# Performance work log

Measured on AMD Instinct MI355X. Metric: run time of the kernel, lower is better.

The kernel has to match this reference:

```python
import jax, jax.numpy as jnp
import numpy as np
from jax import lax

B, C, HW = 256, 3, 64
D, K, LAT = 256, 8192, 128  # embedding_dim, num_embeddings, latent per head
EPS = 1e-5
SLOPE = 0.01  # LeakyReLU default
DN = ('NCHW', 'OIHW', 'NCHW')

def _conv(x, w, b, s, p):
    y = lax.conv_general_dilated(x, w, (s, s), ((p, p), (p, p)), dimension_numbers=DN)
    return y + b[None, :, None, None]

def _convT(x, w, b, s, p, op):
    # PyTorch ConvTranspose2d weight is (Cin, Cout, kh, kw): flip spatial, swap io.
    wt = jnp.flip(w, (2, 3)).transpose(1, 0, 2, 3)
    lo = w.shape[2] - 1 - p
    y = lax.conv_general_dilated(x, wt, (1, 1), ((lo, lo + op), (lo, lo + op)),
                                 lhs_dilation=(s, s), dimension_numbers=DN)
    return y + b[None, :, None, None]

def _bn(x):
    # training-mode BatchNorm2d with default affine init (gamma=1, beta=0)
    mu = jnp.mean(x, (0, 2, 3), keepdims=True)
    var = jnp.var(x, (0, 2, 3), keepdims=True)
    return (x - mu) * lax.rsqrt(var + EPS)

def _lrelu(x):
    return jnp.where(x >= 0, x, SLOPE * x)

def _forward(x, enc_w1, enc_b1, enc_w2, enc_b2, enc_w3, enc_b3, enc_w4, enc_b4,
             enc_wmu, enc_bmu, enc_wcov, enc_bcov, codebook,
             dec_wfc, dec_bfc, dec_wt1, dec_bt1, dec_wt2, dec_bt2,
             dec_wt3, dec_bt3, dec_wt31, dec_bt31, dec_wt4, dec_bt4):
    # ---- Encoder ----
    h = _bn(_lrelu(_conv(x, enc_w1, enc_b1, 2, 1)))   # [B,32,32,32]
    h = _bn(_lrelu(_conv(h, enc_w2, enc_b2, 2, 1)))   # [B,64,16,16]
    h = _bn(_lrelu(_conv(h, enc_w3, enc_b3, 2, 1)))   # [B,128,8,8]
    h = _bn(_lrelu(_conv(h, enc_w4, enc_b4, 2, 1)))   # [B,256,4,4]
    h = h.reshape(h.shape[0], -1)                     # [B,4096]
    mu = h @ enc_wmu.T + enc_bmu                      # [B,LAT]
    cov = jax.nn.relu(h @ enc_wcov.T + enc_bcov)      # [B,LAT]
    z_e = jnp.concatenate([mu, cov], axis=1)          # [B,D]
    # ---- VQ: pairwise L2 -> argmin -> gather ----
    d2 = (jnp.sum(z_e * z_e, 1, keepdims=True)
          + jnp.sum(codebook * codebook, 1)[None, :]
          - 2.0 * (z_e @ codebook.T))                 # [B,K]
    idx = jnp.argmin(d2, axis=1)                      # [B]
    z_q = codebook[idx]                               # [B,D]
    sg = lax.stop_gradient
    emb_loss = jnp.sum((sg(z_e) - z_q) ** 2)
    com_loss = jnp.sum((z_e - sg(z_q)) ** 2)
    vq_loss = emb_loss + com_loss
    z_q_st = z_e + sg(z_q - z_e)                      # straight-through
    # ---- Decoder ----
    g = (z_q_st @ dec_wfc.T + dec_bfc).reshape(-1, 256, 4, 4)
    g = _bn(_lrelu(_convT(g, dec_wt1, dec_bt1, 2, 1, 1)))    # [B,128,8,8]
    g = _bn(_lrelu(_convT(g, dec_wt2, dec_bt2, 2, 1, 1)))    # [B,64,16,16]
    g = _bn(_lrelu(_convT(g, dec_wt3, dec_bt3, 2, 1, 1)))    # [B,32,32,32]
    g = _bn(_lrelu(_convT(g, dec_wt31, dec_bt31, 2, 1, 1)))  # [B,32,64,64]
    out = jnp.tanh(_convT(g, dec_wt4, dec_bt4, 1, 1, 0))     # [B,3,64,64]
    x_hat = 0.5 + 0.5 * out
    return x_hat, vq_loss

def setup_inputs() -> dict:
    key = jax.random.key(0)
    ks = iter(jax.random.split(key, 40))
    def n(shape, s=0.05):
        return (jax.random.normal(next(ks), shape) * s).astype(jnp.float32)
    FC_IN = 256 * 4 * 4
    inp = {
        'x': jax.random.normal(next(ks), (B, C, HW, HW), dtype=jnp.float32),
        'enc_w1': n((32, C, 3, 3)), 'enc_b1': n((32,)),
        'enc_w2': n((64, 32, 3, 3)), 'enc_b2': n((64,)),
        'enc_w3': n((128, 64, 3, 3)), 'enc_b3': n((128,)),
        'enc_w4': n((256, 128, 3, 3)), 'enc_b4': n((256,)),
        'enc_wmu': n((LAT, FC_IN), 0.02), 'enc_bmu': n((LAT,)),
        'enc_wcov': n((LAT, FC_IN), 0.02), 'enc_bcov': n((LAT,)),
        'codebook': jax.random.uniform(next(ks), (K, D), jnp.float32, -1.0 / K, 1.0 / K),
        'dec_wfc': n((FC_IN, D), 0.02), 'dec_bfc': n((FC_IN,)),
        'dec_wt1': n((256, 128, 3, 3)), 'dec_bt1': n((128,)),
        'dec_wt2': n((128, 64, 3, 3)), 'dec_bt2': n((64,)),
        'dec_wt3': n((64, 32, 3, 3)), 'dec_bt3': n((32,)),
        'dec_wt31': n((32, 32, 3, 3)), 'dec_bt31': n((32,)),
        'dec_wt4': n((32, C, 3, 3)), 'dec_bt4': n((C,)),
    }
    return inp

def reference(x, enc_w1, enc_b1, enc_w2, enc_b2, enc_w3, enc_b3, enc_w4, enc_b4,
              enc_wmu, enc_bmu, enc_wcov, enc_bcov, codebook,
              dec_wfc, dec_bfc, dec_wt1, dec_bt1, dec_wt2, dec_bt2,
              dec_wt3, dec_bt3, dec_wt31, dec_bt31, dec_wt4, dec_bt4):
    return _forward(x, enc_w1, enc_b1, enc_w2, enc_b2, enc_w3, enc_b3, enc_w4, enc_b4,
                    enc_wmu, enc_bmu, enc_wcov, enc_bcov, codebook,
                    dec_wfc, dec_bfc, dec_wt1, dec_bt1, dec_wt2, dec_bt2,
                    dec_wt3, dec_bt3, dec_wt31, dec_bt31, dec_wt4, dec_bt4)
```

## Files before the change

kernel.cpp:

```cpp
#include <hip/hip_runtime.h>
#include <cmath>


#define EPS_BN 1e-5f
typedef unsigned short ushort;
typedef short short8 __attribute__((ext_vector_type(8)));
typedef ushort us4 __attribute__((ext_vector_type(4)));
typedef float f32x4 __attribute__((ext_vector_type(4)));

__device__ __forceinline__ float lrelu(float v) { return v >= 0.f ? v : 0.01f * v; }
__device__ __forceinline__ ushort f2bf(float f) {
  unsigned u = __float_as_uint(f);
  return (ushort)((u + 0x7FFF + ((u >> 16) & 1)) >> 16);
}
__device__ __forceinline__ float bf2f(ushort u) {
  return __uint_as_float(((unsigned)u) << 16);
}

__global__ __launch_bounds__(256) void tr_convw_bf(const float* __restrict__ w,
                                                   ushort* __restrict__ wT,
                                                   int CIN, int COUT, int total) {
  int i = blockIdx.x * 256 + threadIdx.x;
  if (i >= total) return;
  int co = i / (9 * CIN);
  int r = i - co * 9 * CIN;
  int t = r / CIN, ci = r - t * CIN;
  wT[i] = f2bf(w[((size_t)co * CIN + ci) * 9 + t]);
}

__global__ __launch_bounds__(256) void tr_convtw_bf(const float* __restrict__ w,
                                                    ushort* __restrict__ wT,
                                                    int CIN, int COUT, int total) {
  int i = blockIdx.x * 256 + threadIdx.x;
  if (i >= total) return;
  const int cc = CIN * COUT;
  int p, base, Kp;
  if (i < cc) { p = 0; base = 0; Kp = CIN; }
  else if (i < 3 * cc) { p = 1; base = cc; Kp = 2 * CIN; }
  else if (i < 5 * cc) { p = 2; base = 3 * cc; Kp = 2 * CIN; }
  else { p = 3; base = 5 * cc; Kp = 4 * CIN; }
  const int r = i - base;
  const int co = r / Kp;
  const int q = r - co * Kp;
  const int tix = q / CIN, ci = q - (q / CIN) * CIN;
  const int py = p >> 1, px = p & 1;
  const int nx = px ? 2 : 1;
  const int kyi = tix / nx, kxi = tix - kyi * nx;
  const int ky = py ? (kyi == 0 ? 0 : 2) : 1;
  const int kx = px ? (kxi == 0 ? 0 : 2) : 1;
  wT[i] = f2bf(w[((size_t)ci * COUT + co) * 9 + ky * 3 + kx]);
}

__global__ __launch_bounds__(256) void tr_convtw_tc(const float* __restrict__ w,
                                                    ushort* __restrict__ wT,
                                                    int CIN, int COUT, int total) {
  int i = blockIdx.x * 256 + threadIdx.x;
  if (i >= total) return;
  int ci = i % CIN;
  int tmp = i / CIN;
  int co = tmp % COUT;
  int t = tmp / COUT;
  const int co_slot = ((co & 1) << 4) | (co >> 1);
  wT[((size_t)t * COUT + co_slot) * CIN + ci] =
      f2bf(w[((size_t)ci * COUT + co) * 9 + t]);
}

__global__ __launch_bounds__(256) void tr_w4(const float* __restrict__ w,
                                             ushort* __restrict__ wT) {
  int i = blockIdx.x * 256 + threadIdx.x;
  if (i >= 4608) return;
  const int s = i >> 9;
  const int l = (i >> 3) & 63;
  const int j = i & 7;
  const int nn = l & 15;
  const int ci = ((l >> 4) << 3) + j;
  const int ty = s / 3, tx = s - ty * 3;
  ushort v = 0;
  if (nn < 3)
    v = f2bf(w[((size_t)ci * 3 + nn) * 9 + (2 - ty) * 3 + (2 - tx)]);
  wT[i] = v;
}

__global__ __launch_bounds__(256) void tr_w1b(const float* __restrict__ w,
                                              ushort* __restrict__ wT) {
  int i = blockIdx.x * 256 + threadIdx.x;
  if (i >= 1024) return;
  const int j = i & 7, l = (i >> 3) & 63, f = i >> 9;
  const int c = 2 * (l & 15) + f;
  const int k = ((l >> 4) << 3) + j;
  ushort v = 0;
  if (k < 27) {
    const int ci = k / 9, r = k - ci * 9;
    v = f2bf(w[((size_t)c * 3 + ci) * 9 + r]);
  }
  wT[i] = v;
}

__global__ __launch_bounds__(256) void tr_a4(const float* __restrict__ in,
                                             float* __restrict__ out) {
  int i = blockIdx.x * 256 + threadIdx.x;
  int n = i >> 12, k = i & 4095;
  out[i] = in[(size_t)(n << 12) + ((k & 15) << 8) + (k >> 4)];
}

__global__ __launch_bounds__(256) void tr_fcdec(const float* __restrict__ in,
                                                const float* __restrict__ bin,
                                                float* __restrict__ out,
                                                float* __restrict__ bout) {
  int i = blockIdx.x * 256 + threadIdx.x;
  int k = i >> 8, d = i & 255;
  int kp = (k & 15) * 256 + (k >> 4);
  out[(size_t)kp * 256 + d] = in[i];
  if (d == 0) bout[kp] = bin[k];
}

template <int TN, int MODE, int IH, int CIN, int COUT, bool HASN, bool INBF>
__global__ __launch_bounds__(256) void mfmaconv(
    const float* __restrict__ X, const ushort* __restrict__ WT,
    const float* __restrict__ bias, const float* __restrict__ st, float invN,
    float* __restrict__ Y, float* __restrict__ stOut) {
  constexpr int OH = (MODE == 0) ? IH / 2 : 2 * IH;
  constexpr int NF = TN / 16;
  __shared__ short As[2][64][40];
  __shared__ short Bs[2][TN][40];
  __shared__ float nrm0[HASN ? CIN : 4], nrm1[HASN ? CIN : 4];
  __shared__ float redS[4][TN], redQ[4][TN];
  const int tid = threadIdx.x;
  const int wv = tid >> 6, lane = tid & 63;
  const int quad = lane >> 4, ln15 = tid & 15;
  if (HASN) {
    for (int c = tid; c < CIN; c += 256) {
      float m = st[c] * invN;
      float var = st[256 + c] * invN - m * m;
      float s = rsqrtf(var + EPS_BN);
      nrm0[c] = s;
      nrm1[c] = m * s;
    }
    __syncthreads();
  }
  int py = 0, px = 0, nx = 1, K = 9 * CIN;
  const ushort* W = WT;
  if (MODE == 1) {
    const int pz = blockIdx.z;
    py = pz >> 1;
    px = pz & 1;
    nx = px ? 2 : 1;
    const int ny = py ? 2 : 1;
    K = ny * nx * CIN;
    const int pre[4] = {0, 1, 3, 5};
    W = WT + (size_t)pre[pz] * CIN * COUT;
  }
  const int gyTM = blockIdx.y * 64;
  const int gxTN = blockIdx.x * TN;

  const int sm = tid & 63, skg = (tid >> 6) * 8;
  const int bn = tid >> 2, bkg = (tid & 3) * 8;
  int baseNB, baseIY, baseIX;
  {
    const int gm = gyTM + sm;
    if (MODE == 0) {
      const int ni = gm / (OH * OH), r = gm % (OH * OH);
      baseNB = ni * IH * IH;
      baseIY = 2 * (r / OH) - 1;
      baseIX = 2 * (r % OH) - 1;
    } else {
      const int ni = gm / (IH * IH), r = gm % (IH * IH);
      baseNB = ni * IH * IH;
      baseIY = r / IH;
      baseIX = r % IH;
    }
  }
  f32x4 acc[NF];
#pragma unroll
  for (int f = 0; f < NF; ++f) acc[f] = (f32x4){0.f, 0.f, 0.f, 0.f};

  const int nsteps = K / 32;

  {
    int iy, ix;
    if (MODE == 0) {
      iy = baseIY;
      ix = baseIX;
    } else {
      iy = baseIY + (py ? 1 : 0);
      ix = baseIX + (px ? 1 : 0);
    }
    const bool ok =
        ((unsigned)iy < (unsigned)IH) && ((unsigned)ix < (unsigned)IH);
    float v[8] = {0.f, 0.f, 0.f, 0.f, 0.f, 0.f, 0.f, 0.f};
    if (ok) {
      if constexpr (INBF) {
        const ushort* xp =
            (const ushort*)X + ((size_t)baseNB + iy * IH + ix) * CIN + skg;
        const short8 raw = *(const short8*)xp;
#pragma unroll
        for (int u = 0; u < 8; ++u) v[u] = bf2f((ushort)raw[u]);
      } else {
        const float* xp = &X[((size_t)baseNB + iy * IH + ix) * CIN + skg];
        const float4 va = *(const float4*)xp, vb = *(const float4*)(xp + 4);
        v[0] = va.x; v[1] = va.y; v[2] = va.z; v[3] = va.w;
        v[4] = vb.x; v[5] = vb.y; v[6] = vb.z; v[7] = vb.w;
      }
      if (HASN) {
#pragma unroll
        for (int u = 0; u < 8; ++u)
          v[u] = fmaf(v[u], nrm0[skg + u], -nrm1[skg + u]);
      }
    }
    short8 o;
#pragma unroll
    for (int u = 0; u < 8; ++u) o[u] = (short)f2bf(v[u]);
    *(short8*)&As[0][sm][skg] = o;
    if (tid < TN * 4)
      *(short8*)&Bs[0][bn][bkg] =
          *(const short8*)&W[(size_t)(gxTN + bn) * K + bkg];
  }
  __syncthreads();

  for (int kk = 0; kk < nsteps; ++kk) {
    const int cur = kk & 1, nxt = cur ^ 1;

    bool okN = false;
    int ci0N = 0;
    short8 rawN;
    float4 vaN, vbN;
    short8 rawBN;
    const bool hasNext = (kk + 1 < nsteps);
    if (hasNext) {
      const int k0n = (kk + 1) * 32;
      const int t = k0n / CIN;
      ci0N = k0n - t * CIN;
      int iy, ix;
      if (MODE == 0) {
        iy = baseIY + t / 3;
        ix = baseIX + (t - (t / 3) * 3);
      } else {
        const int kyi = t / nx, kxi = t - (t / nx) * nx;
        iy = baseIY + ((py && kyi == 0) ? 1 : 0);
        ix = baseIX + ((px && kxi == 0) ? 1 : 0);
      }
      okN = ((unsigned)iy < (unsigned)IH) && ((unsigned)ix < (unsigned)IH);
      if (okN) {
        if constexpr (INBF) {
          const ushort* xp = (const ushort*)X +
                             ((size_t)baseNB + iy * IH + ix) * CIN + ci0N + skg;
          rawN = *(const short8*)xp;
        } else {
          const float* xp =
              &X[((size_t)baseNB + iy * IH + ix) * CIN + ci0N + skg];
          vaN = *(const float4*)xp;
          vbN = *(const float4*)(xp + 4);
        }
      }
      if (tid < TN * 4)
        rawBN = *(const short8*)&W[(size_t)(gxTN + bn) * K + k0n + bkg];
    }

    const short8 a = *(const short8*)&As[cur][wv * 16 + ln15][quad * 8];
#pragma unroll
    for (int f = 0; f < NF; ++f) {
      const short8 b = *(const short8*)&Bs[cur][f * 16 + ln15][quad * 8];
      acc[f] = __builtin_amdgcn_mfma_f32_16x16x32_bf16(a, b, acc[f], 0, 0, 0);
    }

    if (hasNext) {
      float v[8] = {0.f, 0.f, 0.f, 0.f, 0.f, 0.f, 0.f, 0.f};
      if (okN) {
        if constexpr (INBF) {
#pragma unroll
          for (int u = 0; u < 8; ++u) v[u] = bf2f((ushort)rawN[u]);
        } else {
          v[0] = vaN.x; v[1] = vaN.y; v[2] = vaN.z; v[3] = vaN.w;
          v[4] = vbN.x; v[5] = vbN.y; v[6] = vbN.z; v[7] = vbN.w;
        }
        if (HASN) {
          const int c = ci0N + skg;
#pragma unroll
          for (int u = 0; u < 8; ++u)
            v[u] = fmaf(v[u], nrm0[c + u], -nrm1[c + u]);
        }
      }
      short8 o;
#pragma unroll
      for (int u = 0; u < 8; ++u) o[u] = (short)f2bf(v[u]);
      *(short8*)&As[nxt][sm][skg] = o;
      if (tid < TN * 4) *(short8*)&Bs[nxt][bn][bkg] = rawBN;
    }
    __syncthreads();
  }

  size_t maddr[4];
#pragma unroll
  for (int r = 0; r < 4; ++r) {
    const int m = gyTM + wv * 16 + quad * 4 + r;
    if (MODE == 0) {
      const int ni = m / (OH * OH), rr = m % (OH * OH);
      maddr[r] = (((size_t)ni * OH + rr / OH) * OH + rr % OH) * COUT;
    } else {
      const int ni = m / (IH * IH), rr = m % (IH * IH);
      const int oy = 2 * (rr / IH) + py, ox = 2 * (rr % IH) + px;
      maddr[r] = (((size_t)ni * OH + oy) * OH + ox) * COUT;
    }
  }
#pragma unroll
  for (int f = 0; f < NF; ++f) {
    const int col = gxTN + f * 16 + ln15;
    const float bv = bias[col];
    float cS = 0.f, cQ = 0.f;
#pragma unroll
    for (int r = 0; r < 4; ++r) {
      const float o = lrelu(acc[f][r] + bv);
      cS += o;
      cQ += o * o;
      Y[maddr[r] + col] = o;
    }
    cS += __shfl_down(cS, 32); cS += __shfl_down(cS, 16);
    cQ += __shfl_down(cQ, 32); cQ += __shfl_down(cQ, 16);
    if (lane < 16) { redS[wv][f * 16 + ln15] = cS; redQ[wv][f * 16 + ln15] = cQ; }
  }
  __syncthreads();
  if (tid < TN) {
    float S = redS[0][tid] + redS[1][tid] + redS[2][tid] + redS[3][tid];
    float Q = redQ[0][tid] + redQ[1][tid] + redQ[2][tid] + redQ[3][tid];
    atomicAdd(&stOut[gxTN + tid], S);
    atomicAdd(&stOut[256 + gxTN + tid], Q);
  }
}

__global__ __launch_bounds__(256) void gemm_bf_abt(
    const float* __restrict__ A, const float* __restrict__ B,
    const float* __restrict__ bias, float* __restrict__ C, int K, int N,
    float alpha) {
  __shared__ short As[2][64][40];
  __shared__ short Bs[2][64][40];
  const int tid = threadIdx.x;
  const int wv = tid >> 6, lane = tid & 63;
  const int quad = lane >> 4, ln15 = lane & 15;
  const int gm0 = blockIdx.y * 64, gn0 = blockIdx.x * 64;
  const int sm = tid & 63, skg = (tid >> 6) * 8;
  const int bn = tid >> 2, bkg = (tid & 3) * 8;
  const float* Ap = A + (size_t)(gm0 + sm) * K + skg;
  const float* Bp = B + (size_t)(gn0 + bn) * K + bkg;
  f32x4 acc[4];
#pragma unroll
  for (int f = 0; f < 4; ++f) acc[f] = (f32x4){0.f, 0.f, 0.f, 0.f};
  const int nsteps = K / 32;

  {
    const float4 va = *(const float4*)Ap, vb = *(const float4*)(Ap + 4);
    short8 o;
    o[0] = (short)f2bf(va.x); o[1] = (short)f2bf(va.y);
    o[2] = (short)f2bf(va.z); o[3] = (short)f2bf(va.w);
    o[4] = (short)f2bf(vb.x); o[5] = (short)f2bf(vb.y);
    o[6] = (short)f2bf(vb.z); o[7] = (short)f2bf(vb.w);
    *(short8*)&As[0][sm][skg] = o;
    const float4 wa = *(const float4*)Bp, wb = *(const float4*)(Bp + 4);
    short8 p;
    p[0] = (short)f2bf(wa.x); p[1] = (short)f2bf(wa.y);
    p[2] = (short)f2bf(wa.z); p[3] = (short)f2bf(wa.w);
    p[4] = (short)f2bf(wb.x); p[5] = (short)f2bf(wb.y);
    p[6] = (short)f2bf(wb.z); p[7] = (short)f2bf(wb.w);
    *(short8*)&Bs[0][bn][bkg] = p;
  }
  __syncthreads();

  for (int kk = 0; kk < nsteps; ++kk) {
    const int cur = kk & 1, nxt = cur ^ 1;
    const bool hasNext = (kk + 1 < nsteps);
    float4 vaN, vbN, waN, wbN;
    if (hasNext) {
      const int k0n = (kk + 1) * 32;
      vaN = *(const float4*)(Ap + k0n);
      vbN = *(const float4*)(Ap + k0n + 4);
      waN = *(const float4*)(Bp + k0n);
      wbN = *(const float4*)(Bp + k0n + 4);
    }

    const short8 a = *(const short8*)&As[cur][wv * 16 + ln15][quad * 8];
#pragma unroll
    for (int f = 0; f < 4; ++f) {
      const short8 b = *(const short8*)&Bs[cur][f * 16 + ln15][quad * 8];
      acc[f] = __builtin_amdgcn_mfma_f32_16x16x32_bf16(a, b, acc[f], 0, 0, 0);
    }

    if (hasNext) {
      short8 o;
      o[0] = (short)f2bf(vaN.x); o[1] = (short)f2bf(vaN.y);
      o[2] = (short)f2bf(vaN.z); o[3] = (short)f2bf(vaN.w);
      o[4] = (short)f2bf(vbN.x); o[5] = (short)f2bf(vbN.y);
      o[6] = (short)f2bf(vbN.z); o[7] = (short)f2bf(vbN.w);
      *(short8*)&As[nxt][sm][skg] = o;
      short8 p;
      p[0] = (short)f2bf(waN.x); p[1] = (short)f2bf(waN.y);
      p[2] = (short)f2bf(waN.z); p[3] = (short)f2bf(waN.w);
      p[4] = (short)f2bf(wbN.x); p[5] = (short)f2bf(wbN.y);
      p[6] = (short)f2bf(wbN.z); p[7] = (short)f2bf(wbN.w);
      *(short8*)&Bs[nxt][bn][bkg] = p;
    }
    __syncthreads();
  }

#pragma unroll
  for (int f = 0; f < 4; ++f) {
    const int col = gn0 + f * 16 + ln15;
    const float bv = bias[col];
#pragma unroll
    for (int r = 0; r < 4; ++r) {
      const int row = gm0 + wv * 16 + quad * 4 + r;
      C[(size_t)row * N + col] = fmaf(alpha, acc[f][r], bv);
    }
  }
}

template <int IH, int CIN, bool HASN, bool INBF, int NSTRIP>
__global__ __launch_bounds__(256) void convt_mfma(
    const float* __restrict__ X, const ushort* __restrict__ WT,
    const float* __restrict__ bias, const float* __restrict__ st, float invN,
    float* __restrict__ Y, float* __restrict__ stOut) {
  constexpr int OH = 2 * IH;
  constexpr int L = (IH == 32) ? 5 : 4;
  constexpr int RSPAN = 64 / IH;
  constexpr int NP = (RSPAN + 1) * (IH + 1);
  constexpr int LK = CIN + 8;
  constexpr int TI = NP * (CIN / 8);
  constexpr int ITER = (TI + 255) / 256;
  __shared__ short As[2][NP][LK];
  __shared__ short Ws[9 * 32][LK];
  __shared__ float nrm0[HASN ? CIN : 4], nrm1[HASN ? CIN : 4];
  __shared__ float redS[4][32], redQ[4][32];
  const int tid = threadIdx.x;
  const int wv = tid >> 6, lane = tid & 63;
  const int quad = lane >> 4, ln15 = lane & 15;
  if (HASN) {
    for (int c = tid; c < CIN; c += 256) {
      float m = st[c] * invN;
      float var = st[256 + c] * invN - m * m;
      float s = rsqrtf(var + EPS_BN);
      nrm0[c] = s;
      nrm1[c] = m * s;
    }
  }
  for (int i = tid; i < 9 * 32 * (CIN / 8); i += 256) {
    const int row = i / (CIN / 8), kg = (i % (CIN / 8)) * 8;
    *(short8*)&Ws[row][kg] = *(const short8*)&WT[(size_t)row * CIN + kg];
  }
  __syncthreads();

  const int strip0 = blockIdx.x * NSTRIP;
  const int n = (strip0 * 64) / (IH * IH);
  const int iy0base = (strip0 * 64 - n * (IH * IH)) >> L;

#pragma unroll
  for (int it = 0; it < ITER; ++it) {
    const int i = tid + it * 256;
    if (i < TI) {
      const int slot = i / (CIN / 8), kg = (i % (CIN / 8)) * 8;
      const int ty = slot / (IH + 1), tx = slot - ty * (IH + 1);
      const int iy = iy0base + ty;
      short8 o = {0, 0, 0, 0, 0, 0, 0, 0};
      if (iy < IH && tx < IH) {
        float v[8];
        if constexpr (INBF) {
          const ushort* xp =
              (const ushort*)X + (((size_t)n * IH + iy) * IH + tx) * CIN + kg;
          const short8 raw = *(const short8*)xp;
#pragma unroll
          for (int u = 0; u < 8; ++u) v[u] = bf2f((ushort)raw[u]);
        } else {
          const float* xp = &X[(((size_t)n * IH + iy) * IH + tx) * CIN + kg];
          const float4 va = *(const float4*)xp, vb = *(const float4*)(xp + 4);
          v[0] = va.x; v[1] = va.y; v[2] = va.z; v[3] = va.w;
          v[4] = vb.x; v[5] = vb.y; v[6] = vb.z; v[7] = vb.w;
        }
        if (HASN) {
#pragma unroll
          for (int u = 0; u < 8; ++u)
            v[u] = fmaf(v[u], nrm0[kg + u], -nrm1[kg + u]);
        }
#pragma unroll
        for (int u = 0; u < 8; ++u) o[u] = (short)f2bf(v[u]);
      }
      *(short8*)&As[0][slot][kg] = o;
    }
  }
  __syncthreads();

  const int rA = wv * 16 + ln15;
  const int baseIdx = (rA >> L) * (IH + 1) + (rA & (IH - 1));
  constexpr int NT[4] = {4, 2, 2, 1};
  constexpr int TT[4][4] = {{4, 5, 7, 8}, {3, 6, 0, 0}, {1, 2, 0, 0}, {0, 0, 0, 0}};
  const float bv0 = bias[2 * ln15], bv1 = bias[2 * ln15 + 1];
  unsigned* Yp = (unsigned*)Y;
  float cS[2] = {0.f, 0.f}, cQ[2] = {0.f, 0.f};

#pragma unroll
  for (int s = 0; s < NSTRIP; ++s) {
    const int cur = s & 1, nxt = cur ^ 1;
    const int iy0 = iy0base + s * RSPAN;

    short8 rbf[ITER];
    float4 rva[ITER], rvb[ITER];
    bool vld[ITER];
    if (s + 1 < NSTRIP) {
      const int iyN0 = iy0 + RSPAN;
#pragma unroll
      for (int it = 0; it < ITER; ++it) {
        vld[it] = false;
        const int i = tid + it * 256;
        if (i < TI) {
          const int slot = i / (CIN / 8), kg = (i % (CIN / 8)) * 8;
          const int ty = slot / (IH + 1), tx = slot - ty * (IH + 1);
          const int iy = iyN0 + ty;
          if (iy < IH && tx < IH) {
            vld[it] = true;
            if constexpr (INBF) {
              const ushort* xp = (const ushort*)X +
                                 (((size_t)n * IH + iy) * IH + tx) * CIN + kg;
              rbf[it] = *(const short8*)xp;
            } else {
              const float* xp =
                  &X[(((size_t)n * IH + iy) * IH + tx) * CIN + kg];
              rva[it] = *(const float4*)xp;
              rvb[it] = *(const float4*)(xp + 4);
            }
          }
        }
      }
    }

    f32x4 acc[4][2];
#pragma unroll
    for (int p = 0; p < 4; ++p)
#pragma unroll
      for (int f = 0; f < 2; ++f) acc[p][f] = (f32x4){0.f, 0.f, 0.f, 0.f};
#pragma unroll
    for (int sh = 0; sh < 4; ++sh) {
      const int off = (sh >> 1) * (IH + 1) + (sh & 1);
#pragma unroll
      for (int j = 0; j < NT[sh]; ++j) {
        const int t = TT[sh][j];
        const int ky = t / 3, kx = t - ky * 3;
        const int par = ((ky == 1) ? 0 : 2) + ((kx == 1) ? 0 : 1);
#pragma unroll
        for (int ks = 0; ks < CIN / 32; ++ks) {
          const short8 a =
              *(const short8*)&As[cur][baseIdx + off][ks * 32 + quad * 8];
#pragma unroll
          for (int f = 0; f < 2; ++f) {
            const short8 b =
                *(const short8*)&Ws[t * 32 + f * 16 + ln15][ks * 32 + quad * 8];
            acc[par][f] = __builtin_amdgcn_mfma_f32_16x16x32_bf16(
                a, b, acc[par][f], 0, 0, 0);
          }
        }
      }
    }

#pragma unroll
    for (int i = 0; i < 4; ++i) {
      const int rD = wv * 16 + quad * 4 + i;
      const int ry = rD >> L, rx = rD & (IH - 1);
      const int iy = iy0 + ry;
#pragma unroll
      for (int p = 0; p < 4; ++p) {
        const int a = p >> 1, b = p & 1;
        const size_t base =
            (((size_t)n * OH + 2 * iy + a) * OH + 2 * rx + b) * 32;
        const float o0 = lrelu(acc[p][0][i] + bv0);
        const float o1 = lrelu(acc[p][1][i] + bv1);
        cS[0] += o0; cQ[0] += o0 * o0;
        cS[1] += o1; cQ[1] += o1 * o1;
        Yp[(base >> 1) + ln15] = (unsigned)f2bf(o0) | ((unsigned)f2bf(o1) << 16);
      }
    }

    if (s + 1 < NSTRIP) {
#pragma unroll
      for (int it = 0; it < ITER; ++it) {
        const int i = tid + it * 256;
        if (i < TI) {
          const int slot = i / (CIN / 8), kg = (i % (CIN / 8)) * 8;
          short8 o = {0, 0, 0, 0, 0, 0, 0, 0};
          if (vld[it]) {
            float v[8];
            if constexpr (INBF) {
#pragma unroll
              for (int u = 0; u < 8; ++u) v[u] = bf2f((ushort)rbf[it][u]);
            } else {
              v[0] = rva[it].x; v[1] = rva[it].y;
              v[2] = rva[it].z; v[3] = rva[it].w;
              v[4] = rvb[it].x; v[5] = rvb[it].y;
              v[6] = rvb[it].z; v[7] = rvb[it].w;
            }
            if (HASN) {
#pragma unroll
              for (int u = 0; u < 8; ++u)
                v[u] = fmaf(v[u], nrm0[kg + u], -nrm1[kg + u]);
            }
#pragma unroll
            for (int u = 0; u < 8; ++u) o[u] = (short)f2bf(v[u]);
          }
          *(short8*)&As[nxt][slot][kg] = o;
        }
      }
    }
    __syncthreads();
  }

#pragma unroll
  for (int f = 0; f < 2; ++f) {
    float s_ = cS[f], q_ = cQ[f];
    s_ += __shfl_down(s_, 32); s_ += __shfl_down(s_, 16);
    q_ += __shfl_down(q_, 32); q_ += __shfl_down(q_, 16);
    if (lane < 16) { redS[wv][f * 16 + ln15] = s_; redQ[wv][f * 16 + ln15] = q_; }
  }
  __syncthreads();
  if (tid < 32) {
    float S = redS[0][tid] + redS[1][tid] + redS[2][tid] + redS[3][tid];
    float Q = redQ[0][tid] + redQ[1][tid] + redQ[2][tid] + redQ[3][tid];
    const int ch = ((tid & 15) << 1) | (tid >> 4);
    atomicAdd(&stOut[ch], S);
    atomicAdd(&stOut[256 + ch], Q);
  }
}

__global__ __launch_bounds__(256) void conv1_mfma(
    const float* __restrict__ x, const ushort* __restrict__ WT,
    const float* __restrict__ bias, ushort* __restrict__ y,
    float* __restrict__ st) {
  __shared__ float xin[3][17][67];
  __shared__ float redS[4][32], redQ[4][32];
  const int tid = threadIdx.x;
  const int wv = tid >> 6, lane = tid & 63;
  const int quad = lane >> 4, ln15 = lane & 15;
  const short8 bf0 = *(const short8*)&WT[(size_t)lane * 8];
  const short8 bf1 = *(const short8*)&WT[(size_t)(64 + lane) * 8];
  const int n = blockIdx.x >> 2;
  const int oy0 = (blockIdx.x & 3) * 8;
  const int iy0 = 2 * oy0 - 1;
  if (tid < 51) {
    const int ci = tid / 17, r = tid - ci * 17;
    xin[ci][r][0] = 0.f;
  }
  for (int i = tid; i < 816; i += 256) {
    const int ci = i / 272;
    const int r = (i - ci * 272) >> 4;
    const int c4 = (i & 15) << 2;
    const int iy = iy0 + r;
    float4 v = make_float4(0.f, 0.f, 0.f, 0.f);
    if ((unsigned)iy < 64u)
      v = *(const float4*)&x[((size_t)(n * 3 + ci) * 64 + iy) * 64 + c4];
    xin[ci][r][1 + c4] = v.x;
    xin[ci][r][2 + c4] = v.y;
    xin[ci][r][3 + c4] = v.z;
    xin[ci][r][4 + c4] = v.w;
  }
  __syncthreads();

  const float bv0 = bias[2 * ln15], bv1 = bias[2 * ln15 + 1];
  unsigned* Yp = (unsigned*)y;
  float cS[2] = {0.f, 0.f}, cQ[2] = {0.f, 0.f};
#pragma unroll
  for (int rr = 0; rr < 2; ++rr) {
    const int row = 2 * wv + rr;
#pragma unroll
    for (int h = 0; h < 2; ++h) {
      short8 a;
#pragma unroll
      for (int j = 0; j < 8; ++j) {
        const int k = quad * 8 + j;
        float val = 0.f;
        if (k < 27) {
          const int ci = k / 9, r2 = k - ci * 9;
          const int ky = r2 / 3, kx = r2 - ky * 3;
          val = xin[ci][2 * row + ky][2 * (h * 16 + ln15) + kx];
        }
        a[j] = (short)f2bf(val);
      }
      f32x4 acc0 = (f32x4){0.f, 0.f, 0.f, 0.f};
      f32x4 acc1 = (f32x4){0.f, 0.f, 0.f, 0.f};
      acc0 = __builtin_amdgcn_mfma_f32_16x16x32_bf16(a, bf0, acc0, 0, 0, 0);
      acc1 = __builtin_amdgcn_mfma_f32_16x16x32_bf16(a, bf1, acc1, 0, 0, 0);
#pragma unroll
      for (int r = 0; r < 4; ++r) {
        const int px = h * 16 + quad * 4 + r;
        const float o0 = lrelu(acc0[r] + bv0);
        const float o1 = lrelu(acc1[r] + bv1);
        cS[0] += o0; cQ[0] += o0 * o0;
        cS[1] += o1; cQ[1] += o1 * o1;
        Yp[((size_t)n * 1024 + (oy0 + row) * 32 + px) * 16 + ln15] =
            (unsigned)f2bf(o0) | ((unsigned)f2bf(o1) << 16);
      }
    }
  }
#pragma unroll
  for (int f = 0; f < 2; ++f) {
    float s_ = cS[f], q_ = cQ[f];
    s_ += __shfl_down(s_, 32); s_ += __shfl_down(s_, 16);
    q_ += __shfl_down(q_, 32); q_ += __shfl_down(q_, 16);
    if (lane < 16) { redS[wv][f * 16 + ln15] = s_; redQ[wv][f * 16 + ln15] = q_; }
  }
  __syncthreads();
  if (tid < 32) {
    float S = redS[0][tid] + redS[1][tid] + redS[2][tid] + redS[3][tid];
    float Q = redQ[0][tid] + redQ[1][tid] + redQ[2][tid] + redQ[3][tid];
    const int ch = ((tid & 15) << 1) | (tid >> 4);
    atomicAdd(&st[ch], S);
    atomicAdd(&st[256 + ch], Q);
  }
}

__global__ __launch_bounds__(256) void convt4_mfma(
    const float* __restrict__ X, const ushort* __restrict__ WT,
    const float* __restrict__ bias, const float* __restrict__ st, float invN,
    float* __restrict__ out) {
  __shared__ short ring[4][66][32];
  __shared__ float s0[32], s1[32];
  const int tid = threadIdx.x;
  const int wv = tid >> 6, lane = tid & 63;
  const int quad = lane >> 4, ln15 = lane & 15;
  if (tid < 32) {
    float m = st[tid] * invN;
    float var = st[256 + tid] * invN - m * m;
    float s = rsqrtf(var + EPS_BN);
    s0[tid] = s;
    s1[tid] = m * s;
  }
  if (tid >= 32 && tid < 64) {
    const int t = tid - 32;
    const int slot = t >> 3, h = (t >> 2) & 1, kg = (t & 3) * 8;
    short8 z = {0, 0, 0, 0, 0, 0, 0, 0};
    *(short8*)&ring[slot][h ? 65 : 0][kg] = z;
  }
  short8 bfrag[9];
#pragma unroll
  for (int s = 0; s < 9; ++s)
    bfrag[s] = *(const short8*)&WT[((size_t)s * 64 + lane) * 8];
  __syncthreads();

  const int n = blockIdx.x >> 2;
  const int y0 = (blockIdx.x & 3) * 16;
  const ushort* xn = (const ushort*)X + (size_t)n * 131072;
  const int spx = tid >> 2, skg = (tid & 3) * 8;

#pragma unroll
  for (int pr = 0; pr < 3; ++pr) {
    const int Y = y0 - 1 + pr;
    short8 o = {0, 0, 0, 0, 0, 0, 0, 0};
    if ((unsigned)Y < 64u) {
      const short8 raw = *(const short8*)&xn[((size_t)Y * 64 + spx) * 32 + skg];
#pragma unroll
      for (int u = 0; u < 8; ++u)
        o[u] = (short)f2bf(fmaf(bf2f((ushort)raw[u]), s0[skg + u], -s1[skg + u]));
    }
    *(short8*)&ring[Y & 3][spx + 1][skg] = o;
  }
  __syncthreads();

  const int x0 = wv * 16;
  const float bv = (ln15 < 3) ? bias[ln15] : 0.f;
  float* op = out + (size_t)n * 3 * 4096;

  for (int y = y0; y < y0 + 16; ++y) {
    const int Ypf = y + 2;
    const bool pre = (Ypf <= y0 + 16);
    short8 raw;
    bool vld = false;
    if (pre && (unsigned)Ypf < 64u) {
      raw = *(const short8*)&xn[((size_t)Ypf * 64 + spx) * 32 + skg];
      vld = true;
    }

    f32x4 acc0 = (f32x4){0.f, 0.f, 0.f, 0.f};
    f32x4 acc1 = (f32x4){0.f, 0.f, 0.f, 0.f};
#pragma unroll
    for (int ty = 0; ty < 3; ++ty) {
      const short* rp = &ring[(y - 1 + ty) & 3][0][0];
#pragma unroll
      for (int tx = 0; tx < 3; ++tx) {
        const short8 a = *(const short8*)&rp[(x0 + ln15 + tx) * 32 + quad * 8];
        const int s = ty * 3 + tx;
        if (s & 1)
          acc1 = __builtin_amdgcn_mfma_f32_16x16x32_bf16(a, bfrag[s], acc1, 0, 0, 0);
        else
          acc0 = __builtin_amdgcn_mfma_f32_16x16x32_bf16(a, bfrag[s], acc0, 0, 0, 0);
      }
    }

    if (ln15 < 3) {
      float4 o;
      float v;
      v = acc0[0] + acc1[0] + bv; o.x = 1.f / (1.f + __expf(-2.f * v));
      v = acc0[1] + acc1[1] + bv; o.y = 1.f / (1.f + __expf(-2.f * v));
      v = acc0[2] + acc1[2] + bv; o.z = 1.f / (1.f + __expf(-2.f * v));
      v = acc0[3] + acc1[3] + bv; o.w = 1.f / (1.f + __expf(-2.f * v));
      *(float4*)&op[(size_t)ln15 * 4096 + y * 64 + x0 + quad * 4] = o;
    }

    if (pre) {
      short8 o = {0, 0, 0, 0, 0, 0, 0, 0};
      if (vld) {
#pragma unroll
        for (int u = 0; u < 8; ++u)
          o[u] = (short)f2bf(
              fmaf(bf2f((ushort)raw[u]), s0[skg + u], -s1[skg + u]));
      }
      *(short8*)&ring[Ypf & 3][spx + 1][skg] = o;
    }
    __syncthreads();
  }
}

__global__ __launch_bounds__(256) void gemm_abt(
    const float* __restrict__ A, const float* __restrict__ B,
    const float* __restrict__ bias, const float* __restrict__ stA, float invN,
    float* __restrict__ C, float* __restrict__ P, int K, int ldc, int col0,
    float alpha, int act) {
  __shared__ float As[16][68];
  __shared__ float Bsh[16][68];
  __shared__ float nrm[2][256];
  const int tid = threadIdx.x;
  if (stA) {
    const int c = tid;
    float m = stA[c] * invN;
    float var = stA[256 + c] * invN - m * m;
    float s = rsqrtf(var + EPS_BN);
    nrm[0][c] = s;
    nrm[1][c] = m * s;
    __syncthreads();
  }
  const int lm = tid >> 2, lk = (tid & 3) << 2;
  const int KS = gridDim.z;
  const int kChunk = K / KS;
  const int kStart = blockIdx.z * kChunk;
  const float* Arow = A + (size_t)(blockIdx.y * 64 + lm) * K + lk;
  const float* Brow = B + (size_t)(blockIdx.x * 64 + lm) * K + lk;
  float acc[4][4] = {};
  const int m0 = (tid >> 4) << 2, n0 = (tid & 15) << 2;

  for (int k0 = kStart; k0 < kStart + kChunk; k0 += 16) {
    float4 av = *(const float4*)(Arow + k0);
    float4 bv = *(const float4*)(Brow + k0);
    if (stA) {
      const int ch = (k0 + lk) >> 4;
      const float s = nrm[0][ch], ms = nrm[1][ch];
      av.x = fmaf(av.x, s, -ms);
      av.y = fmaf(av.y, s, -ms);
      av.z = fmaf(av.z, s, -ms);
      av.w = fmaf(av.w, s, -ms);
    }
    As[lk + 0][lm] = av.x; As[lk + 1][lm] = av.y;
    As[lk + 2][lm] = av.z; As[lk + 3][lm] = av.w;
    Bsh[lk + 0][lm] = bv.x; Bsh[lk + 1][lm] = bv.y;
    Bsh[lk + 2][lm] = bv.z; Bsh[lk + 3][lm] = bv.w;
    __syncthreads();
#pragma unroll
    for (int kk = 0; kk < 16; ++kk) {
      const float4 a = *(const float4*)&As[kk][m0];
      const float4 b = *(const float4*)&Bsh[kk][n0];
      acc[0][0] = fmaf(a.x, b.x, acc[0][0]); acc[0][1] = fmaf(a.x, b.y, acc[0][1]);
      acc[0][2] = fmaf(a.x, b.z, acc[0][2]); acc[0][3] = fmaf(a.x, b.w, acc[0][3]);
      acc[1][0] = fmaf(a.y, b.x, acc[1][0]); acc[1][1] = fmaf(a.y, b.y, acc[1][1]);
      acc[1][2] = fmaf(a.y, b.z, acc[1][2]); acc[1][3] = fmaf(a.y, b.w, acc[1][3]);
      acc[2][0] = fmaf(a.z, b.x, acc[2][0]); acc[2][1] = fmaf(a.z, b.y, acc[2][1]);
      acc[2][2] = fmaf(a.z, b.z, acc[2][2]); acc[2][3] = fmaf(a.z, b.w, acc[2][3]);
      acc[3][0] = fmaf(a.w, b.x, acc[3][0]); acc[3][1] = fmaf(a.w, b.y, acc[3][1]);
      acc[3][2] = fmaf(a.w, b.z, acc[3][2]); acc[3][3] = fmaf(a.w, b.w, acc[3][3]);
    }
    __syncthreads();
  }

  const int gm = blockIdx.y * 64 + m0;
  const int gn = blockIdx.x * 64 + n0;
  if (KS == 1) {
#pragma unroll
    for (int i = 0; i < 4; ++i) {
      float4 o;
      o.x = alpha * acc[i][0] + bias[gn + 0];
      o.y = alpha * acc[i][1] + bias[gn + 1];
      o.z = alpha * acc[i][2] + bias[gn + 2];
      o.w = alpha * acc[i][3] + bias[gn + 3];
      if (act == 1) {
        o.x = fmaxf(o.x, 0.f); o.y = fmaxf(o.y, 0.f);
        o.z = fmaxf(o.z, 0.f); o.w = fmaxf(o.w, 0.f);
      }
      *(float4*)&C[(size_t)(gm + i) * ldc + col0 + gn] = o;
    }
  } else {
    const int M = gridDim.y * 64, N = gridDim.x * 64;
#pragma unroll
    for (int i = 0; i < 4; ++i)
      *(float4*)&P[((size_t)blockIdx.z * M + gm + i) * N + gn] =
          make_float4(acc[i][0], acc[i][1], acc[i][2], acc[i][3]);
  }
}

__global__ __launch_bounds__(256) void gemm_reduce(
    const float* __restrict__ P, float* __restrict__ C,
    const float* __restrict__ bias, int M, int N, int ldc, int col0,
    float alpha, int act, int KS) {
  const int idx = blockIdx.x * 256 + threadIdx.x;
  if (idx >= M * N) return;
  const int m = idx / N, n = idx % N;
  float s = 0.f;
  for (int z = 0; z < KS; ++z) s += P[((size_t)z * M + m) * N + n];
  float v = alpha * s + bias[n];
  if (act == 1) v = fmaxf(v, 0.f);
  C[(size_t)m * ldc + col0 + n] = v;
}

__global__ __launch_bounds__(256) void rowsq(const float* __restrict__ cb,
                                             float* __restrict__ csq) {
  const int row = blockIdx.x * 4 + (threadIdx.x >> 6);
  const int ln = threadIdx.x & 63;
  const float4 v = ((const float4*)(cb + (size_t)row * 256))[ln];
  float s = v.x * v.x + v.y * v.y + v.z * v.z + v.w * v.w;
#pragma unroll
  for (int off = 32; off > 0; off >>= 1) s += __shfl_down(s, off);
  if (ln == 0) csq[row] = s;
}

__global__ __launch_bounds__(256) void argmin_d2(const float* __restrict__ d2,
                                                 int* __restrict__ idx) {
  const int b = blockIdx.x, t = threadIdx.x;
  const float* row = d2 + (size_t)b * 8192;
  float best = 3.4e38f;
  int bi = 0x7fffffff;
  for (int k = t; k < 8192; k += 256) {
    const float v = row[k];
    if (v < best) { best = v; bi = k; }
  }
  __shared__ float bval[256];
  __shared__ int bidx[256];
  bval[t] = best;
  bidx[t] = bi;
  __syncthreads();
  for (int s = 128; s > 0; s >>= 1) {
    if (t < s) {
      const float ov = bval[t + s];
      const int oi = bidx[t + s];
      if (ov < bval[t] || (ov == bval[t] && oi < bidx[t])) {
        bval[t] = ov;
        bidx[t] = oi;
      }
    }
    __syncthreads();
  }
  if (t == 0) idx[b] = bidx[0];
}

__global__ __launch_bounds__(256) void vq_gather_loss(
    const float* __restrict__ ze, const float* __restrict__ cb,
    const int* __restrict__ idx, float* __restrict__ zq,
    float* __restrict__ lossacc) {
  const int b = blockIdx.x, d = threadIdx.x;
  const int i = b * 256 + d;
  const float q = cb[(size_t)idx[b] * 256 + d];
  zq[i] = q;
  const float df = ze[i] - q;
  float v = df * df;
  __shared__ float sh[256];
  sh[d] = v;
  __syncthreads();
  for (int s = 128; s > 0; s >>= 1) {
    if (d < s) sh[d] += sh[d + s];
    __syncthreads();
  }
  if (d == 0) atomicAdd(lossacc, sh[0]);
}

__global__ void write_loss(const float* __restrict__ lossacc,
                           float* __restrict__ out) {
  out[0] = 2.f * lossacc[0];
}

extern "C" void kernel_launch(void* const* d_in, const int* in_sizes, int n_in,
                              void* d_out, int out_size, void* d_ws,
                              size_t ws_size, hipStream_t stream) {
  const float* x = (const float*)d_in[0];
  const float* ew1 = (const float*)d_in[1];
  const float* eb1 = (const float*)d_in[2];
  const float* ew2 = (const float*)d_in[3];
  const float* eb2 = (const float*)d_in[4];
  const float* ew3 = (const float*)d_in[5];
  const float* eb3 = (const float*)d_in[6];
  const float* ew4 = (const float*)d_in[7];
  const float* eb4 = (const float*)d_in[8];
  const float* wmu = (const float*)d_in[9];
  const float* bmu = (const float*)d_in[10];
  const float* wcov = (const float*)d_in[11];
  const float* bcov = (const float*)d_in[12];
  const float* cb = (const float*)d_in[13];
  const float* wfc = (const float*)d_in[14];
  const float* bfc = (const float*)d_in[15];
  const float* wt1 = (const float*)d_in[16];
  const float* bt1 = (const float*)d_in[17];
  const float* wt2 = (const float*)d_in[18];
  const float* bt2 = (const float*)d_in[19];
  const float* wt3 = (const float*)d_in[20];
  const float* bt3 = (const float*)d_in[21];
  const float* wt31 = (const float*)d_in[22];
  const float* bt31 = (const float*)d_in[23];
  const float* wt4 = (const float*)d_in[24];
  const float* bt4 = (const float*)d_in[25];

  float* ws = (float*)d_ws;
  float* a1 = ws;
  float* a2 = a1 + 8388608;
  float* a3 = a2 + 4194304;
  float* a4 = a3 + 2097152;
  float* g31 = a4 + 1048576;
  float* d2 = g31;
  float* P = g31 + 2097152;
  float* csq = g31 + 2359296;
  float* a4n = g31 + 2367488;
  float* wfcT = g31 + 3416064;
  float* bfcT = g31 + 4464640;
  ushort* wTc2 = (ushort*)(g31 + 4468736);
  ushort* wTc3 = (ushort*)(g31 + 4487168);
  ushort* wTc4 = (ushort*)(g31 + 4560896);
  float* ze = g31 + 33554432;
  float* zq = ze + 65536;
  float* stats = zq + 65536;
  float* lossacc = stats + 4096;
  int* idx = (int*)(lossacc + 4);
  ushort* wTt1 = (ushort*)(lossacc + 4 + 256);
  ushort* wTt2 = wTt1 + 294912;
  ushort* wTt3 = wTt2 + 73728;
  ushort* wTt31 = wTt3 + 18432;
  ushort* wT4 = wTt31 + 9216;
  ushort* wb1 = wT4 + 4608;
  float* g3 = a1;
  float* g2 = a2;
  float* g1 = a3;
  float* g0 = a4;

  float* st0 = stats + 0 * 512;
  float* st1 = stats + 1 * 512;
  float* st2 = stats + 2 * 512;
  float* st3 = stats + 3 * 512;
  float* st4 = stats + 4 * 512;
  float* st5 = stats + 5 * 512;
  float* st6 = stats + 6 * 512;
  float* st7 = stats + 7 * 512;

  hipMemsetAsync(stats, 0, (4096 + 8) * sizeof(float), stream);

  tr_convw_bf<<<72, 256, 0, stream>>>(ew2, wTc2, 32, 64, 18432);
  tr_convw_bf<<<288, 256, 0, stream>>>(ew3, wTc3, 64, 128, 73728);
  tr_convw_bf<<<1152, 256, 0, stream>>>(ew4, wTc4, 128, 256, 294912);
  tr_convtw_bf<<<1152, 256, 0, stream>>>(wt1, wTt1, 256, 128, 294912);
  tr_convtw_bf<<<288, 256, 0, stream>>>(wt2, wTt2, 128, 64, 73728);
  tr_convtw_tc<<<72, 256, 0, stream>>>(wt3, wTt3, 64, 32, 18432);
  tr_convtw_tc<<<36, 256, 0, stream>>>(wt31, wTt31, 32, 32, 9216);
  tr_w4<<<18, 256, 0, stream>>>(wt4, wT4);
  tr_w1b<<<4, 256, 0, stream>>>(ew1, wb1);
  tr_fcdec<<<4096, 256, 0, stream>>>(wfc, bfc, wfcT, bfcT);
  rowsq<<<2048, 256, 0, stream>>>(cb, csq);

  conv1_mfma<<<1024, 256, 0, stream>>>(x, wb1, eb1, (ushort*)a1, st0);
  mfmaconv<64, 0, 32, 32, 64, true, true><<<dim3(1, 1024), 256, 0, stream>>>(
      a1, wTc2, eb2, st0, 1.f / (256.f * 1024.f), a2, st1);
  mfmaconv<64, 0, 16, 64, 128, true, false><<<dim3(2, 256), 256, 0, stream>>>(
      a2, wTc3, eb3, st1, 1.f / (256.f * 256.f), a3, st2);
  mfmaconv<64, 0, 8, 128, 256, true, false><<<dim3(4, 64), 256, 0, stream>>>(
      a3, wTc4, eb4, st2, 1.f / (256.f * 64.f), a4, st3);
  tr_a4<<<4096, 256, 0, stream>>>(a4, a4n);

  gemm_abt<<<dim3(2, 4, 8), 256, 0, stream>>>(a4n, wmu, nullptr, st3,
                                              1.f / 4096.f, nullptr, P, 4096,
                                              0, 0, 1.f, 0);
  gemm_reduce<<<128, 256, 0, stream>>>(P, ze, bmu, 256, 128, 256, 0, 1.f, 0, 8);
  gemm_abt<<<dim3(2, 4, 8), 256, 0, stream>>>(a4n, wcov, nullptr, st3,
                                              1.f / 4096.f, nullptr, P, 4096,
                                              0, 0, 1.f, 0);
  gemm_reduce<<<128, 256, 0, stream>>>(P, ze, bcov, 256, 128, 256, 128, 1.f, 1, 8);

  gemm_bf_abt<<<dim3(128, 4), 256, 0, stream>>>(ze, cb, csq, d2, 256, 8192,
                                                -2.f);
  argmin_d2<<<256, 256, 0, stream>>>(d2, idx);
  vq_gather_loss<<<256, 256, 0, stream>>>(ze, cb, idx, zq, lossacc);

  gemm_bf_abt<<<dim3(64, 4), 256, 0, stream>>>(zq, wfcT, bfcT, g0, 256, 4096,
                                               1.f);

  mfmaconv<64, 1, 4, 256, 128, false, false><<<dim3(2, 64, 4), 256, 0, stream>>>(
      g0, wTt1, bt1, nullptr, 0.f, g1, st4);
  mfmaconv<64, 1, 8, 128, 64, true, false><<<dim3(1, 256, 4), 256, 0, stream>>>(
      g1, wTt2, bt2, st4, 1.f / (256.f * 64.f), g2, st5);
  convt_mfma<16, 64, true, false, 2><<<512, 256, 0, stream>>>(
      g2, wTt3, bt3, st5, 1.f / (256.f * 256.f), g3, st6);
  convt_mfma<32, 32, true, true, 4><<<1024, 256, 0, stream>>>(
      g3, wTt31, bt31, st6, 1.f / (256.f * 1024.f), g31, st7);

  convt4_mfma<<<1024, 256, 0, stream>>>(g31, wT4, bt4, st7,
                                        1.f / (256.f * 4096.f), (float*)d_out);
  write_loss<<<1, 1, 0, stream>>>(lossacc, (float*)d_out + 3145728);
}
```

Baseline: 505.1 us.

## Store intermediate conv activations as bf16 with permuted output channels

Adds an OUTBF epilogue to mfmaconv that writes four adjacent channels per lane as packed bf16. To make those channels contiguous, the weight transpose kernels permute output-channel slots. Several encoder and decoder layers now produce bf16 outputs and read bf16 inputs, which halves activation memory traffic. The convt_mfma launches also change their per-block batch factor and grid size. The risk is layout inconsistency between producers and consumers, plus the precision loss from bf16 storage.

Result: slower. 661.6 us (+31.0%).

```diff
diff --git a/kernel.cpp b/kernel.cpp
--- a/kernel.cpp
+++ b/kernel.cpp
@@ -19,13 +19,19 @@
 
 __global__ __launch_bounds__(256) void tr_convw_bf(const float* __restrict__ w,
                                                    ushort* __restrict__ wT,
-                                                   int CIN, int COUT, int total) {
+                                                   int CIN, int COUT, int total,
+                                                   int perm) {
   int i = blockIdx.x * 256 + threadIdx.x;
   if (i >= total) return;
   int co = i / (9 * CIN);
   int r = i - co * 9 * CIN;
   int t = r / CIN, ci = r - t * CIN;
-  wT[i] = f2bf(w[((size_t)co * CIN + ci) * 9 + t]);
+  int co_s = co;
+  if (perm) {
+    const int cr = co & 63;
+    co_s = (co - cr) + ((cr & 3) << 4) + (cr >> 2);
+  }
+  wT[(size_t)co_s * 9 * CIN + r] = f2bf(w[((size_t)co * CIN + ci) * 9 + t]);
 }
 
 __global__ __launch_bounds__(256) void tr_convtw_bf(const float* __restrict__ w,
@@ -48,7 +54,10 @@
   const int kyi = tix / nx, kxi = tix - kyi * nx;
   const int ky = py ? (kyi == 0 ? 0 : 2) : 1;
   const int kx = px ? (kxi == 0 ? 0 : 2) : 1;
-  wT[i] = f2bf(w[((size_t)ci * COUT + co) * 9 + ky * 3 + kx]);
+  const int cr = co & 63;
+  const int co_s = (co - cr) + ((cr & 3) << 4) + (cr >> 2);
+  wT[base + (size_t)co_s * Kp + q] =
+      f2bf(w[((size_t)ci * COUT + co) * 9 + ky * 3 + kx]);
 }
 
 __global__ __launch_bounds__(256) void tr_convtw_tc(const float* __restrict__ w,
@@ -114,13 +123,15 @@
   if (d == 0) bout[kp] = bin[k];
 }
 
-template <int TN, int MODE, int IH, int CIN, int COUT, bool HASN, bool INBF>
+template <int TN, int MODE, int IH, int CIN, int COUT, bool HASN, bool INBF,
+          bool OUTBF>
 __global__ __launch_bounds__(256) void mfmaconv(
     const float* __restrict__ X, const ushort* __restrict__ WT,
     const float* __restrict__ bias, const float* __restrict__ st, float invN,
     float* __restrict__ Y, float* __restrict__ stOut) {
   constexpr int OH = (MODE == 0) ? IH / 2 : 2 * IH;
   constexpr int NF = TN / 16;
+  static_assert(!OUTBF || NF == 4, "OUTBF requires NF==4");
   __shared__ short As[2][64][40];
   __shared__ short Bs[2][TN][40];
   __shared__ float nrm0[HASN ? CIN : 4], nrm1[HASN ? CIN : 4];
@@ -302,28 +313,66 @@
       maddr[r] = (((size_t)ni * OH + oy) * OH + ox) * COUT;
     }
   }
-#pragma unroll
-  for (int f = 0; f < NF; ++f) {
-    const int col = gxTN + f * 16 + ln15;
-    const float bv = bias[col];
-    float cS = 0.f, cQ = 0.f;
+  if constexpr (OUTBF) {
+    const int ch0 = gxTN + 4 * ln15;
+    const float b0 = bias[ch0 + 0], b1 = bias[ch0 + 1];
+    const float b2 = bias[ch0 + 2], b3 = bias[ch0 + 3];
+    ushort* Yb = (ushort*)Y;
+    float cS[4] = {0.f, 0.f, 0.f, 0.f}, cQ[4] = {0.f, 0.f, 0.f, 0.f};
 #pragma unroll
     for (int r = 0; r < 4; ++r) {
-      const float o = lrelu(acc[f][r] + bv);
-      cS += o;
-      cQ += o * o;
-      Y[maddr[r] + col] = o;
-    }
-    cS += __shfl_down(cS, 32); cS += __shfl_down(cS, 16);
-    cQ += __shfl_down(cQ, 32); cQ += __shfl_down(cQ, 16);
-    if (lane < 16) { redS[wv][f * 16 + ln15] = cS; redQ[wv][f * 16 + ln15] = cQ; }
-  }
-  __syncthreads();
-  if (tid < TN) {
-    float S = redS[0][tid] + redS[1][tid] + redS[2][tid] + redS[3][tid];
-    float Q = redQ[0][tid] + redQ[1][tid] + redQ[2][tid] + redQ[3][tid];
-    atomicAdd(&stOut[gxTN + tid], S);
-    atomicAdd(&stOut[256 + gxTN + tid], Q);
+      const float o0 = lrelu(acc[0][r] + b0);
+      const float o1 = lrelu(acc[1][r] + b1);
+      const float o2 = lrelu(acc[2][r] + b2);
+      const float o3 = lrelu(acc[3][r] + b3);
+      cS[0] += o0; cQ[0] += o0 * o0;
+      cS[1] += o1; cQ[1] += o1 * o1;
+      cS[2] += o2; cQ[2] += o2 * o2;
+      cS[3] += o3; cQ[3] += o3 * o3;
+      uint2 pk;
+      pk.x = (unsigned)f2bf(o0) | ((unsigned)f2bf(o1) << 16);
+      pk.y = (unsigned)f2bf(o2) | ((unsigned)f2bf(o3) << 16);
+      *(uint2*)&Yb[maddr[r] + ch0] = pk;
+    }
+#pragma unroll
+    for (int f = 0; f < 4; ++f) {
+      float s_ = cS[f], q_ = cQ[f];
+      s_ += __shfl_down(s_, 32); s_ += __shfl_down(s_, 16);
+      q_ += __shfl_down(q_, 32); q_ += __shfl_down(q_, 16);
+      if (lane < 16) { redS[wv][f * 16 + ln15] = s_; redQ[wv][f * 16 + ln15] = q_; }
+    }
+    __syncthreads();
+    if (tid < TN) {
+      float S = redS[0][tid] + redS[1][tid] + redS[2][tid] + redS[3][tid];
+      float Q = redQ[0][tid] + redQ[1][tid] + redQ[2][tid] + redQ[3][tid];
+      const int ch = gxTN + 4 * (tid & 15) + (tid >> 4);
+      atomicAdd(&stOut[ch], S);
+      atomicAdd(&stOut[256 + ch], Q);
+    }
+  } else {
+#pragma unroll
+    for (int f = 0; f < NF; ++f) {
+      const int col = gxTN + f * 16 + ln15;
+      const float bv = bias[col];
+      float cS = 0.f, cQ = 0.f;
+#pragma unroll
+      for (int r = 0; r < 4; ++r) {
+        const float o = lrelu(acc[f][r] + bv);
+        cS += o;
+        cQ += o * o;
+        Y[maddr[r] + col] = o;
+      }
+      cS += __shfl_down(cS, 32); cS += __shfl_down(cS, 16);
+      cQ += __shfl_down(cQ, 32); cQ += __shfl_down(cQ, 16);
+      if (lane < 16) { redS[wv][f * 16 + ln15] = cS; redQ[wv][f * 16 + ln15] = cQ; }
+    }
+    __syncthreads();
+    if (tid < TN) {
+      float S = redS[0][tid] + redS[1][tid] + redS[2][tid] + redS[3][tid];
+      float Q = redQ[0][tid] + redQ[1][tid] + redQ[2][tid] + redQ[3][tid];
+      atomicAdd(&stOut[gxTN + tid], S);
+      atomicAdd(&stOut[256 + gxTN + tid], Q);
+    }
   }
 }
 
@@ -1046,9 +1095,9 @@
 
   hipMemsetAsync(stats, 0, (4096 + 8) * sizeof(float), stream);
 
-  tr_convw_bf<<<72, 256, 0, stream>>>(ew2, wTc2, 32, 64, 18432);
-  tr_convw_bf<<<288, 256, 0, stream>>>(ew3, wTc3, 64, 128, 73728);
-  tr_convw_bf<<<1152, 256, 0, stream>>>(ew4, wTc4, 128, 256, 294912);
+  tr_convw_bf<<<72, 256, 0, stream>>>(ew2, wTc2, 32, 64, 18432, 1);
+  tr_convw_bf<<<288, 256, 0, stream>>>(ew3, wTc3, 64, 128, 73728, 1);
+  tr_convw_bf<<<1152, 256, 0, stream>>>(ew4, wTc4, 128, 256, 294912, 0);
   tr_convtw_bf<<<1152, 256, 0, stream>>>(wt1, wTt1, 256, 128, 294912);
   tr_convtw_bf<<<288, 256, 0, stream>>>(wt2, wTt2, 128, 64, 73728);
   tr_convtw_tc<<<72, 256, 0, stream>>>(wt3, wTt3, 64, 32, 18432);
@@ -1059,12 +1108,15 @@
   rowsq<<<2048, 256, 0, stream>>>(cb, csq);
 
   conv1_mfma<<<1024, 256, 0, stream>>>(x, wb1, eb1, (ushort*)a1, st0);
-  mfmaconv<64, 0, 32, 32, 64, true, true><<<dim3(1, 1024), 256, 0, stream>>>(
-      a1, wTc2, eb2, st0, 1.f / (256.f * 1024.f), a2, st1);
-  mfmaconv<64, 0, 16, 64, 128, true, false><<<dim3(2, 256), 256, 0, stream>>>(
-      a2, wTc3, eb3, st1, 1.f / (256.f * 256.f), a3, st2);
-  mfmaconv<64, 0, 8, 128, 256, true, false><<<dim3(4, 64), 256, 0, stream>>>(
-      a3, wTc4, eb4, st2, 1.f / (256.f * 64.f), a4, st3);
+  mfmaconv<64, 0, 32, 32, 64, true, true, true>
+      <<<dim3(1, 1024), 256, 0, stream>>>(a1, wTc2, eb2, st0,
+                                          1.f / (256.f * 1024.f), a2, st1);
+  mfmaconv<64, 0, 16, 64, 128, true, true, true>
+      <<<dim3(2, 256), 256, 0, stream>>>(a2, wTc3, eb3, st1,
+                                         1.f / (256.f * 256.f), a3, st2);
+  mfmaconv<64, 0, 8, 128, 256, true, true, false>
+      <<<dim3(4, 64), 256, 0, stream>>>(a3, wTc4, eb4, st2,
+                                        1.f / (256.f * 64.f), a4, st3);
   tr_a4<<<4096, 256, 0, stream>>>(a4, a4n);
 
   gemm_abt<<<dim3(2, 4, 8), 256, 0, stream>>>(a4n, wmu, nullptr, st3,
@@ -1084,13 +1136,15 @@
   gemm_bf_abt<<<dim3(64, 4), 256, 0, stream>>>(zq, wfcT, bfcT, g0, 256, 4096,
                                                1.f);
 
-  mfmaconv<64, 1, 4, 256, 128, false, false><<<dim3(2, 64, 4), 256, 0, stream>>>(
-      g0, wTt1, bt1, nullptr, 0.f, g1, st4);
-  mfmaconv<64, 1, 8, 128, 64, true, false><<<dim3(1, 256, 4), 256, 0, stream>>>(
-      g1, wTt2, bt2, st4, 1.f / (256.f * 64.f), g2, st5);
-  convt_mfma<16, 64, true, false, 2><<<512, 256, 0, stream>>>(
+  mfmaconv<64, 1, 4, 256, 128, false, false, true>
+      <<<dim3(2, 64, 4), 256, 0, stream>>>(g0, wTt1, bt1, nullptr, 0.f, g1,
+                                           st4);
+  mfmaconv<64, 1, 8, 128, 64, true, true, true>
+      <<<dim3(1, 256, 4), 256, 0, stream>>>(g1, wTt2, bt2, st4,
+                                            1.f / (256.f * 64.f), g2, st5);
+  convt_mfma<16, 64, true, true, 4><<<256, 256, 0, stream>>>(
       g2, wTt3, bt3, st5, 1.f / (256.f * 256.f), g3, st6);
-  convt_mfma<32, 32, true, true, 4><<<1024, 256, 0, stream>>>(
+  convt_mfma<32, 32, true, true, 8><<<512, 256, 0, stream>>>(
       g3, wTt31, bt31, st6, 1.f / (256.f * 1024.f), g31, st7);
 
   convt4_mfma<<<1024, 256, 0, stream>>>(g31, wT4, bt4, st7,
```
